# Performance work log

Hardware: AMD Instinct MI355X
Metric: run time of the kernel (lower is better)

The kernel has to match this reference:

```python
import jax, jax.numpy as jnp
import numpy as np

B, L, K, H = 256, 256, 128, 256


def setup_inputs() -> dict:
    key = jax.random.key(0)
    ks = jax.random.split(key, 24)

    def u(k, shape, fan):
        s = 1.0 / np.sqrt(fan)
        return jax.random.uniform(k, shape, minval=-s, maxval=s, dtype=jnp.float32)

    x = jax.random.normal(ks[0], (B, L, K), jnp.float32)
    mask = (jax.random.uniform(ks[1], (B, L, K)) < 0.7).astype(jnp.float32)
    record_num = jax.random.randint(ks[2], (B,), L // 2, L + 1)
    ts = jnp.cumsum(jax.random.uniform(ks[3], (B, L), minval=0.1, maxval=1.0, dtype=jnp.float32), axis=1)
    time_stamp = ts * (jnp.arange(L)[None, :] < record_num[:, None]).astype(jnp.float32)

    return {
        "x": x,
        "mask": mask,
        "time_stamp": time_stamp,
        # TemporalDecay h: W [H,K], stdv = 1/sqrt(out)=1/sqrt(H)
        "W_gh": u(ks[4], (H, K), H), "b_gh": u(ks[5], (H,), H),
        # TemporalDecay x (diag): W [K,K], stdv = 1/sqrt(K)
        "W_gx": u(ks[6], (K, K), K), "b_gx": u(ks[7], (K,), K),
        # hist_reg: Linear(H -> K), stdv = 1/sqrt(H)
        "W_hist": u(ks[8], (K, H), H), "b_hist": u(ks[9], (K,), H),
        "W_feat": u(ks[10], (K, K), K), "b_feat": u(ks[11], (K,), K),
        # weight_combine: Linear(2K -> K), stdv = 1/sqrt(2K)
        "W_comb": u(ks[12], (K, 2 * K), 2 * K), "b_comb": u(ks[13], (K,), 2 * K),
        # GRUCell(2K -> H): uniform 1/sqrt(H)
        "W_ih": u(ks[14], (3 * H, 2 * K), H), "W_hh": u(ks[15], (3 * H, H), H),
        "b_ih": u(ks[16], (3 * H,), H), "b_hh": u(ks[17], (3 * H,), H),
        # out: Linear(H -> 1)
        "W_out": u(ks[18], (1, H), H), "b_out": u(ks[19], (1,), H),
        "record_num": record_num,
        "direct": 0,
    }


def _forward(x, mask, time_stamp, W_gh, b_gh, W_gx, b_gx, W_hist, b_hist,
             W_feat, b_feat, W_comb, b_comb, W_ih, W_hh, b_ih, b_hh,
             W_out, b_out, record_num):
    Bs, Ls, Ks = x.shape
    Hs = W_gh.shape[0]
    eye = jnp.eye(Ks, dtype=x.dtype)
    W_gx_m = W_gx * eye                 # diag temporal decay
    W_feat_m = W_feat * (1.0 - eye)

    # --- deltas (gen_aux_data): d[0]=1; d[t] = |ts[t]-ts[t-1]| + (1-m[t])*d[t-1] ---
    gaps = jnp.abs(jnp.diff(time_stamp, axis=1))          # [B, L-1]
    mask_t = jnp.swapaxes(mask, 0, 1)                     # [L, B, K]

    def dstep(prev, inp):
        gap, m = inp                                      # [B], [B,K]
        d = gap[:, None] + (1.0 - m) * prev
        return d, d

    d0 = jnp.ones((Bs, Ks), x.dtype)
    _, drest = jax.lax.scan(dstep, d0, (gaps.T, mask_t[1:]))
    deltas = jnp.concatenate([d0[None], drest], axis=0)   # [L, B, K]
    valid = (jnp.arange(Ls)[:, None] < record_num[None, :])  # break at record_num
    deltas = jnp.where(valid[:, :, None], deltas, 0.0)

    evals = (time_stamp != 0).astype(x.dtype)             # [B, L]

    x_t = jnp.swapaxes(x, 0, 1)                           # [L, B, K]
    e_t = evals.T                                         # [L, B]

    def step(carry, inp):
        h, xloss = carry
        xt, mt, dt, et = inp                              # [B,K],[B,K],[B,K],[B]
        e_m = et[:, None]
        gamma_h = jnp.exp(-jax.nn.relu(dt @ W_gh.T + b_gh))   # [B,H]
        gamma_x = jnp.exp(-jax.nn.relu(dt @ W_gx_m.T + b_gx)) # [B,K]
        h_prev = h
        h = h * gamma_h
        x_h = h @ W_hist.T + b_hist
        msum = jnp.sum(mt) + 1e-5
        xloss = xloss + jnp.sum(jnp.abs(xt - x_h) * mt) / msum
        x_c = mt * xt + (1.0 - mt) * x_h
        z_h = x_c @ W_feat_m.T + b_feat
        xloss = xloss + jnp.sum(jnp.abs(xt - z_h) * mt * e_m) / msum
        alpha = jnp.concatenate([gamma_x, mt], axis=1) @ W_comb.T + b_comb
        c_h = alpha * z_h + (1.0 - alpha) * x_h
        xloss = xloss + jnp.sum(jnp.abs(xt - c_h) * mt * e_m) / msum
        c_c = mt * xt + (1.0 - mt) * c_h
        inputs = jnp.concatenate([c_c, mt], axis=1)           # [B, 2K]
        gi = inputs @ W_ih.T + b_ih                           # [B, 3H]
        gh = h @ W_hh.T + b_hh
        ir, iz, ig = jnp.split(gi, 3, axis=1)
        hr, hz, hg = jnp.split(gh, 3, axis=1)
        r = jax.nn.sigmoid(ir + hr)
        z = jax.nn.sigmoid(iz + hz)
        n = jnp.tanh(ig + r * hg)
        h_new = (1.0 - z) * n + z * h
        h_new = h_new * e_m + (1.0 - e_m) * h_prev            # freeze h past record
        return (h_new, xloss), c_c * e_m

    h0 = jnp.zeros((Bs, Hs), x.dtype)
    (h_fin, x_loss), imps = jax.lax.scan(step, (h0, jnp.float32(0.0)), (x_t, mask_t, deltas, e_t))
    imputations = jnp.swapaxes(imps, 0, 1)                # [B, L, K]
    predictions = jax.nn.sigmoid(h_fin @ W_out.T + b_out) # [B, 1]
    return imputations, x_loss, predictions


def reference(x, mask, time_stamp, W_gh, b_gh, W_gx, b_gx, W_hist, b_hist,
              W_feat, b_feat, W_comb, b_comb, W_ih, W_hh, b_ih, b_hh,
              W_out, b_out, record_num, direct):
    return _forward(x, mask, time_stamp, W_gh, b_gh, W_gx, b_gx, W_hist, b_hist,
                    W_feat, b_feat, W_comb, b_comb, W_ih, W_hh, b_ih, b_hh,
                    W_out, b_out, record_num)
```

## Files before the change

### kernel.cpp

```cpp
#include <hip/hip_runtime.h>
#include <math.h>

#define BT 256
#define LT 256
#define KT 128
#define HT 256
#define LOSS_IDX ((size_t)BT*LT*KT)
#define PRED_IDX (LOSS_IDX + 1)
#define LDP 1280
#define GH0 0
#define AL0 256
#define GI0 384
#define ZP0 1152

typedef _Float16 h2 __attribute__((ext_vector_type(2)));
typedef _Float16 f16x8 __attribute__((ext_vector_type(8)));
typedef float f32x4 __attribute__((ext_vector_type(4)));

__device__ __forceinline__ float fd2(h2 a, h2 b, float c){
#if __has_builtin(__builtin_amdgcn_fdot2)
  return __builtin_amdgcn_fdot2(a, b, c, false);
#else
  return c + (float)a[0]*(float)b[0] + (float)a[1]*(float)b[1];
#endif
}
__device__ __forceinline__ float dot8(f16x8 w, f16x8 a, float acc){
  acc = fd2(__builtin_shufflevector(w,w,0,1), __builtin_shufflevector(a,a,0,1), acc);
  acc = fd2(__builtin_shufflevector(w,w,2,3), __builtin_shufflevector(a,a,2,3), acc);
  acc = fd2(__builtin_shufflevector(w,w,4,5), __builtin_shufflevector(a,a,4,5), acc);
  acc = fd2(__builtin_shufflevector(w,w,6,7), __builtin_shufflevector(a,a,6,7), acc);
  return acc;
}
__device__ __forceinline__ float sigf(float v){ return 1.0f/(1.0f + __expf(-v)); }
__device__ __forceinline__ float tanh_fast(float v){
  float a = fminf(fabsf(v), 15.0f);
  float e2 = __expf(2.0f*a);
  float r = (e2 - 1.0f)/(e2 + 1.0f);
  return copysignf(r, v);
}
__device__ __forceinline__ float f16bits(unsigned u, int hi){
  union { unsigned short s; _Float16 h; } c;
  c.s = (unsigned short)(hi ? (u >> 16) : (u & 0xffff));
  return (float)c.h;
}

__global__ void pack_cast(const float* __restrict__ src, _Float16* __restrict__ dst,
                          int J, int Kd, int diag, int total){
  int idx = blockIdx.x*256 + threadIdx.x;
  if (idx >= total) return;
  float v = src[idx];
  if (diag && (idx / Kd) == (idx % Kd)) v = 0.0f;
  dst[idx] = (_Float16)v;
}
__global__ void pack_rowchunks(const float* __restrict__ src, _Float16* __restrict__ dst,
                               int J, int K, int total){
  int idx = blockIdx.x*256 + threadIdx.x;
  if (idx >= total) return;
  int j = idx % J, c = idx / J;
  #pragma unroll
  for (int e = 0; e < 8; ++e)
    dst[(size_t)idx*8 + e] = (_Float16)src[(size_t)j*K + c*8 + e];
}
__global__ void pack_col(const float* __restrict__ src, _Float16* __restrict__ dst,
                         int J, int Kc, int ld, int diag, int total){
  int idx = blockIdx.x*256 + threadIdx.x;
  if (idx >= total) return;
  int j = idx % J, k = idx / J;
  float v = src[(size_t)j*ld + k];
  if (diag && j == k) v = 0.0f;
  dst[idx] = (_Float16)v;
}

__global__ __launch_bounds__(128) void scan_kernel(
    const float* __restrict__ x, const float* __restrict__ mask, const float* __restrict__ ts,
    const float* __restrict__ W_gx, const float* __restrict__ b_gx,
    const int* __restrict__ record_num,
    _Float16* __restrict__ deltas, _Float16* __restrict__ Agx, _Float16* __restrict__ U)
{
  int b = blockIdx.x, k = threadIdx.x;
  int rn = record_num[b];
  float gxd = W_gx[(size_t)k*KT + k];
  float bgx = b_gx[k];
  float d = 1.0f, tsp = 0.0f;
  for (int t0 = 0; t0 < LT; t0 += 8){
    float xv[8], mv[8], tsv[8];
    #pragma unroll
    for (int u = 0; u < 8; ++u){
      size_t off = ((size_t)b*LT + t0 + u)*KT + k;
      xv[u] = x[off]; mv[u] = mask[off];
      tsv[u] = ts[(size_t)b*LT + t0 + u];
    }
    #pragma unroll
    for (int u = 0; u < 8; ++u){
      int t = t0 + u;
      if (t > 0){
        float gap = fabsf(tsv[u] - (u ? tsv[u-1] : tsp));
        d = gap + (1.0f - mv[u])*d;
      }
      float e = (t < rn) ? 1.0f : 0.0f;
      float dev = d * e;
      size_t row = (size_t)b*LT + t;
      deltas[row*KT + k] = (_Float16)dev;
      float gx = __expf(-fmaxf(fmaf(dev, gxd, bgx), 0.0f));
      Agx[row*2*KT + k]      = (_Float16)gx;
      Agx[row*2*KT + KT + k] = (_Float16)mv[u];
      U[row*2*KT + k]        = (_Float16)(mv[u]*xv[u]);
      U[row*2*KT + KT + k]   = (_Float16)mv[u];
    }
    tsp = tsv[7];
  }
}

__global__ void msum_kernel(const float* __restrict__ mask, float* __restrict__ msumInv){
  __shared__ float red[256];
  int t = blockIdx.x;
  float acc = 0.0f;
  for (int i = threadIdx.x; i < BT*KT; i += 256){
    int b = i >> 7, k = i & 127;
    acc += mask[((size_t)b*LT + t)*KT + k];
  }
  red[threadIdx.x] = acc; __syncthreads();
  for (int s = 128; s > 0; s >>= 1){
    if (threadIdx.x < s) red[threadIdx.x] += red[threadIdx.x + s];
    __syncthreads();
  }
  if (threadIdx.x == 0) msumInv[t] = 1.0f/(red[0] + 1e-5f);
}

__global__ __launch_bounds__(256) void gemm_f16(
    const _Float16* __restrict__ A, long ldA, int K,
    const _Float16* __restrict__ B, long ldB,
    _Float16* __restrict__ C, long colofs,
    const float* __restrict__ bias, int op)
{
  const int w = threadIdx.x >> 6, lane = threadIdx.x & 63;
  const int ml = lane & 15, quad = lane >> 4;
  const long m0 = (long)blockIdx.x*64 + w*16;
  const long nb0 = (long)blockIdx.y*64;
  f32x4 acc[4] = {{0,0,0,0},{0,0,0,0},{0,0,0,0},{0,0,0,0}};
  for (int kc = 0; kc < K; kc += 32){
    f16x8 a = *(const f16x8*)(A + (m0 + ml)*ldA + kc + quad*8);
    #pragma unroll
    for (int nt = 0; nt < 4; ++nt){
      f16x8 bfr = *(const f16x8*)(B + (nb0 + nt*16 + ml)*ldB + kc + quad*8);
      acc[nt] = __builtin_amdgcn_mfma_f32_16x16x32_f16(a, bfr, acc[nt], 0, 0, 0);
    }
  }
  #pragma unroll
  for (int nt = 0; nt < 4; ++nt){
    long col = nb0 + nt*16 + ml;
    float bv = (op >= 1) ? bias[col] : 0.0f;
    #pragma unroll
    for (int r = 0; r < 4; ++r){
      float v = acc[nt][r];
      if (op >= 1) v += bv;
      if (op == 2) v = __expf(-fmaxf(v, 0.0f));
      long row = m0 + quad*4 + r;
      C[row*LDP + colofs + col] = (_Float16)v;
    }
  }
}

#define NT 768

struct __align__(16) SeqS {
  float h[HT];
  float hs[HT];
  alignas(16) _Float16 hsh[HT];
  float gh[3*HT];
  float gi[3*HT];
  float xh[KT];
  float part[6][KT];
  float v3[KT], v5[KT];
  int lidx[KT];
  int posk[KT];
  int cnt;
  unsigned pb[2][LDP/2];
  float xb[2][KT], mb[2][KT];
  float bhist[KT], bfeat[KT];
  float bhh[3*HT];
  float wout[HT];
  float red[NT/64];
};

__global__ __launch_bounds__(NT, 1) void rits_seq(
    const float* __restrict__ x, const float* __restrict__ mask,
    const int* __restrict__ record_num, const float* __restrict__ msumInv,
    const _Float16* __restrict__ P,
    const f16x8* __restrict__ Whh_p, const f16x8* __restrict__ Whist_p,
    const _Float16* __restrict__ Wfc, const _Float16* __restrict__ Wihc,
    const float* __restrict__ b_hist, const float* __restrict__ b_feat,
    const float* __restrict__ b_hh,
    const float* __restrict__ W_out, const float* __restrict__ b_out,
    float* __restrict__ out)
{
  __shared__ SeqS s;
  const int tid = threadIdx.x;
  const int b = blockIdx.x;
  const int rn = record_num[b];
  const unsigned* __restrict__ Pd = (const unsigned*)P + (size_t)b*LT*(LDP/2);

  if (tid < HT) s.h[tid] = 0.0f;
  if (tid < KT){ s.bhist[tid] = b_hist[tid]; s.bfeat[tid] = b_feat[tid]; }
  if (tid < 3*HT) s.bhh[tid] = b_hh[tid];
  if (tid >= 256 && tid < 512) s.wout[tid - 256] = W_out[tid - 256];
  if (tid < LDP/2) s.pb[0][tid] = Pd[tid];
  else if (tid < LDP/2 + KT){
    int k = tid - LDP/2;
    s.xb[0][k] = x[((size_t)b*LT)*KT + k];
    s.mb[0][k] = mask[((size_t)b*LT)*KT + k];
  }
  __syncthreads();

  float loss = 0.0f;

  for (int t = 0; t < LT; ++t){
    const int cur = t & 1, nxt = cur ^ 1;

    unsigned pr0 = 0; float prx = 0.0f, prm = 0.0f;
    if (t < LT - 1){
      if (tid < LDP/2) pr0 = Pd[(size_t)(t+1)*(LDP/2) + tid];
      else if (tid < LDP/2 + KT){
        int k = tid - LDP/2;
        size_t off = ((size_t)b*LT + t + 1)*KT + k;
        prx = x[off]; prm = mask[off];
      }
    }

    if (tid == 0) s.cnt = 0;
    if (tid < HT){
      float g = f16bits(s.pb[cur][GH0/2 + (tid >> 1)], tid & 1);
      float hsv = s.h[tid] * g;
      s.hs[tid] = hsv;
      s.hsh[tid] = (_Float16)hsv;
    }
    __syncthreads();

    {
      const f16x8* hp = (const f16x8*)s.hsh;
      float acc = 0.0f;
      #pragma unroll 4
      for (int c = 0; c < 32; ++c)
        acc = dot8(Whh_p[c*768 + tid], hp[c], acc);
      s.gh[tid] = acc;
      if (tid < KT){
        float a2 = 0.0f;
        #pragma unroll 4
        for (int c = 0; c < 32; ++c)
          a2 = dot8(Whist_p[c*KT + tid], hp[c], a2);
        float xh = a2 + s.bhist[tid];
        s.xh[tid] = xh;
        float mv = s.mb[cur][tid], xv = s.xb[cur][tid];
        loss += fabsf(xv - xh) * mv * msumInv[t];
        if (mv == 0.0f){
          int pp = atomicAdd(&s.cnt, 1);
          s.lidx[pp] = tid; s.v3[pp] = xh; s.posk[tid] = pp;
        }
      }
    }
    __syncthreads();

    {
      const int st = tid >> 7, j = tid & 127;
      const int c0 = s.cnt;
      float a = 0.0f;
      for (int i = st; i < c0; i += 6)
        a += s.v3[i] * (float)Wfc[s.lidx[i]*KT + j];
      s.part[st][j] = a;
    }
    __syncthreads();
    if (tid < KT){
      const int j = tid;
      float z = f16bits(s.pb[cur][ZP0/2 + (j >> 1)], j & 1) + s.bfeat[j]
              + s.part[0][j] + s.part[1][j] + s.part[2][j]
              + s.part[3][j] + s.part[4][j] + s.part[5][j];
      float al = f16bits(s.pb[cur][AL0/2 + (j >> 1)], j & 1);
      float xh = s.xh[j];
      float mv = s.mb[cur][j], xv = s.xb[cur][j];
      float e = (t < rn) ? 1.0f : 0.0f;
      float inv = msumInv[t];
      float ch = al*z + (1.0f - al)*xh;
      loss += (fabsf(xv - z) + fabsf(xv - ch)) * mv * e * inv;
      float cc = mv*xv + (1.0f - mv)*ch;
      out[((size_t)b*LT + t)*KT + j] = cc * e;
      if (mv == 0.0f) s.v5[s.posk[j]] = ch;
    }
    __syncthreads();

    {
      const int c0 = s.cnt;
      float g = f16bits(s.pb[cur][GI0/2 + (tid >> 1)], tid & 1);
      for (int i = 0; i < c0; ++i)
        g += s.v5[i] * (float)Wihc[s.lidx[i]*768 + tid];
      s.gi[tid] = g;
    }
    __syncthreads();

    if (tid < HT){
      const int j = tid;
      float ir = s.gi[j],        iz = s.gi[HT + j],        ig = s.gi[2*HT + j];
      float hr = s.gh[j] + s.bhh[j];
      float hz = s.gh[HT + j] + s.bhh[HT + j];
      float hg = s.gh[2*HT + j] + s.bhh[2*HT + j];
      float r = sigf(ir + hr);
      float zg = sigf(iz + hz);
      float n = tanh_fast(ig + r*hg);
      float hn = (1.0f - zg)*n + zg*s.hs[j];
      if (t < rn) s.h[j] = hn;
    }
    if (t < LT - 1){
      if (tid < LDP/2) s.pb[nxt][tid] = pr0;
      else if (tid < LDP/2 + KT){
        int k = tid - LDP/2;
        s.xb[nxt][k] = prx; s.mb[nxt][k] = prm;
      }
    }
    __syncthreads();
  }

  #pragma unroll
  for (int off = 32; off; off >>= 1) loss += __shfl_down(loss, off);
  if ((tid & 63) == 0) s.red[tid >> 6] = loss;
  __syncthreads();
  if (tid == 0){
    float tot = 0.0f;
    #pragma unroll
    for (int w = 0; w < NT/64; ++w) tot += s.red[w];
    atomicAdd(&out[LOSS_IDX], tot);
  }

  if (tid < HT) s.part[0][tid & 127] = 0.0f;
  if (tid < HT) s.gh[tid] = s.h[tid] * s.wout[tid];
  __syncthreads();
  for (int st2 = 128; st2 > 0; st2 >>= 1){
    if (tid < st2) s.gh[tid] += s.gh[tid + st2];
    __syncthreads();
  }
  if (tid == 0) out[PRED_IDX + b] = sigf(s.gh[0] + b_out[0]);
}

extern "C" void kernel_launch(void* const* d_in, const int* in_sizes, int n_in,
                              void* d_out, int out_size, void* d_ws, size_t ws_size,
                              hipStream_t stream){
  const float* x      = (const float*)d_in[0];
  const float* mask   = (const float*)d_in[1];
  const float* ts     = (const float*)d_in[2];
  const float* W_gh   = (const float*)d_in[3];
  const float* b_gh   = (const float*)d_in[4];
  const float* W_gx   = (const float*)d_in[5];
  const float* b_gx   = (const float*)d_in[6];
  const float* W_hist = (const float*)d_in[7];
  const float* b_hist = (const float*)d_in[8];
  const float* W_feat = (const float*)d_in[9];
  const float* b_feat = (const float*)d_in[10];
  const float* W_comb = (const float*)d_in[11];
  const float* b_comb = (const float*)d_in[12];
  const float* W_ih   = (const float*)d_in[13];
  const float* W_hh   = (const float*)d_in[14];
  const float* b_ih   = (const float*)d_in[15];
  const float* b_hh   = (const float*)d_in[16];
  const float* W_out  = (const float*)d_in[17];
  const float* b_out  = (const float*)d_in[18];
  const int*   rn     = (const int*)d_in[19];
  float* out = (float*)d_out;
  char* ws = (char*)d_ws;

  size_t off = 0;
  auto alloc = [&](size_t bytes) -> char* {
    char* p = ws + off;
    off += (bytes + 255) & ~(size_t)255;
    return p;
  };
  _Float16* P      = (_Float16*)alloc((size_t)BT*LT*LDP*2);
  _Float16* deltas = (_Float16*)alloc((size_t)BT*LT*KT*2);
  _Float16* Agx    = (_Float16*)alloc((size_t)BT*LT*2*KT*2);
  _Float16* U      = (_Float16*)alloc((size_t)BT*LT*2*KT*2);
  _Float16* WghF   = (_Float16*)alloc(HT*KT*2);
  _Float16* WcombF = (_Float16*)alloc(KT*2*KT*2);
  _Float16* WihF   = (_Float16*)alloc(3*HT*2*KT*2);
  _Float16* WfeatF = (_Float16*)alloc(KT*KT*2);
  _Float16* Whh_p  = (_Float16*)alloc(3*HT*HT*2);
  _Float16* Whist_p= (_Float16*)alloc(KT*HT*2);
  _Float16* Wfc    = (_Float16*)alloc(KT*KT*2);
  _Float16* Wihc   = (_Float16*)alloc(KT*3*HT*2);
  float* msumInv   = (float*)alloc(LT*4);

  auto grid1 = [](int n){ return dim3((n + 255)/256); };
  pack_cast<<<grid1(HT*KT), 256, 0, stream>>>(W_gh, WghF, HT, KT, 0, HT*KT);
  pack_cast<<<grid1(KT*2*KT), 256, 0, stream>>>(W_comb, WcombF, KT, 2*KT, 0, KT*2*KT);
  pack_cast<<<grid1(3*HT*2*KT), 256, 0, stream>>>(W_ih, WihF, 3*HT, 2*KT, 0, 3*HT*2*KT);
  pack_cast<<<grid1(KT*KT), 256, 0, stream>>>(W_feat, WfeatF, KT, KT, 1, KT*KT);
  pack_rowchunks<<<grid1(3*HT*(HT/8)), 256, 0, stream>>>(W_hh, Whh_p, 3*HT, HT, 3*HT*(HT/8));
  pack_rowchunks<<<grid1(KT*(HT/8)), 256, 0, stream>>>(W_hist, Whist_p, KT, HT, KT*(HT/8));
  pack_col<<<grid1(KT*KT), 256, 0, stream>>>(W_feat, Wfc, KT, KT, KT, 1, KT*KT);
  pack_col<<<grid1(768*KT), 256, 0, stream>>>(W_ih, Wihc, 3*HT, KT, 2*KT, 0, 3*HT*KT);

  scan_kernel<<<dim3(BT), dim3(KT), 0, stream>>>(x, mask, ts, W_gx, b_gx, rn, deltas, Agx, U);
  msum_kernel<<<dim3(LT), dim3(256), 0, stream>>>(mask, msumInv);

  const int MR = BT*LT;
  gemm_f16<<<dim3(MR/64, HT/64), 256, 0, stream>>>(deltas, KT, KT, WghF, KT, P, GH0, b_gh, 2);
  gemm_f16<<<dim3(MR/64, KT/64), 256, 0, stream>>>(Agx, 2*KT, 2*KT, WcombF, 2*KT, P, AL0, b_comb, 1);
  gemm_f16<<<dim3(MR/64, 3*HT/64), 256, 0, stream>>>(U, 2*KT, 2*KT, WihF, 2*KT, P, GI0, b_ih, 1);
  gemm_f16<<<dim3(MR/64, KT/64), 256, 0, stream>>>(U, 2*KT, KT, WfeatF, KT, P, ZP0, (const float*)nullptr, 0);

  hipMemsetAsync((void*)(out + LOSS_IDX), 0, sizeof(float), stream);

  rits_seq<<<dim3(BT), dim3(NT), 0, stream>>>(x, mask, rn, msumInv, P,
      (const f16x8*)Whh_p, (const f16x8*)Whist_p, Wfc, Wihc,
      b_hist, b_feat, b_hh, W_out, b_out, out);
}
```

Baseline: 2.581 ms.

## Stage W_hist and W_feat in LDS and prefetch W_ih gather rows early

Copies the packed W_hist (64KB) and the W_feat fp16 matrix (32KB) into shared memory once per block, so the per-timestep hist and feature-regression dot products read LDS instead of global memory. It also caches msumInv in LDS, moves the W_hh matvec after the W_hist work, and prefetches the first 16 masked W_ih rows into registers before a barrier to hide gather latency. The remaining W_ih gather is unrolled by 8 with zero-padded v5 entries. The much larger LDS footprint and extra registers may lower occupancy, though only one block of 768 threads runs per CU anyway.

New measurement: 2.420 ms. 1.07x faster.

```diff
diff --git a/kernel.cpp b/kernel.cpp
--- a/kernel.cpp
+++ b/kernel.cpp
@@ -164,15 +164,17 @@
 #define NT 768
 
 struct __align__(16) SeqS {
+  f16x8 whist_l[32*128];
+  _Float16 wfc_l[128*128];
   float h[HT];
   float hs[HT];
   alignas(16) _Float16 hsh[HT];
   float gh[3*HT];
   float gi[3*HT];
   float xh[KT];
-  float part[6][KT];
+  float part6[6][KT];
   float v3[KT], v5[KT];
-  int lidx[KT];
+  int lidx[136];
   int posk[KT];
   int cnt;
   unsigned pb[2][LDP/2];
@@ -180,6 +182,7 @@
   float bhist[KT], bfeat[KT];
   float bhh[3*HT];
   float wout[HT];
+  float minv[LT];
   float red[NT/64];
 };
 
@@ -200,10 +203,15 @@
   const int rn = record_num[b];
   const unsigned* __restrict__ Pd = (const unsigned*)P + (size_t)b*LT*(LDP/2);
 
+  for (int i = tid; i < 32*128; i += NT) s.whist_l[i] = Whist_p[i];
+  for (int i = tid; i < 128*128/2; i += NT)
+    ((unsigned*)s.wfc_l)[i] = ((const unsigned*)Wfc)[i];
   if (tid < HT) s.h[tid] = 0.0f;
   if (tid < KT){ s.bhist[tid] = b_hist[tid]; s.bfeat[tid] = b_feat[tid]; }
   if (tid < 3*HT) s.bhh[tid] = b_hh[tid];
+  if (tid < 136) s.lidx[tid] = 0;
   if (tid >= 256 && tid < 512) s.wout[tid - 256] = W_out[tid - 256];
+  if (tid >= 512 && tid < 512 + LT) s.minv[tid - 512] = msumInv[tid - 512];
   if (tid < LDP/2) s.pb[0][tid] = Pd[tid];
   else if (tid < LDP/2 + KT){
     int k = tid - LDP/2;
@@ -220,16 +228,15 @@
     unsigned pr0 = 0; float prx = 0.0f, prm = 0.0f;
     if (t < LT - 1){
       if (tid < LDP/2) pr0 = Pd[(size_t)(t+1)*(LDP/2) + tid];
-      else if (tid < LDP/2 + KT){
+      else {
         int k = tid - LDP/2;
-        size_t off = ((size_t)b*LT + t + 1)*KT + k;
-        prx = x[off]; prm = mask[off];
+        size_t offx = ((size_t)b*LT + t + 1)*KT + k;
+        prx = x[offx]; prm = mask[offx];
       }
     }
-
     if (tid == 0) s.cnt = 0;
     if (tid < HT){
-      float g = f16bits(s.pb[cur][GH0/2 + (tid >> 1)], tid & 1);
+      float g = f16bits(s.pb[cur][tid >> 1], tid & 1);
       float hsv = s.h[tid] * g;
       s.hs[tid] = hsv;
       s.hsh[tid] = (_Float16)hsv;
@@ -238,47 +245,54 @@
 
     {
       const f16x8* hp = (const f16x8*)s.hsh;
-      float acc = 0.0f;
-      #pragma unroll 4
-      for (int c = 0; c < 32; ++c)
-        acc = dot8(Whh_p[c*768 + tid], hp[c], acc);
-      s.gh[tid] = acc;
       if (tid < KT){
         float a2 = 0.0f;
-        #pragma unroll 4
+        #pragma unroll 8
         for (int c = 0; c < 32; ++c)
-          a2 = dot8(Whist_p[c*KT + tid], hp[c], a2);
+          a2 = dot8(s.whist_l[c*128 + tid], hp[c], a2);
         float xh = a2 + s.bhist[tid];
         s.xh[tid] = xh;
         float mv = s.mb[cur][tid], xv = s.xb[cur][tid];
-        loss += fabsf(xv - xh) * mv * msumInv[t];
+        loss += fabsf(xv - xh) * mv * s.minv[t];
         if (mv == 0.0f){
           int pp = atomicAdd(&s.cnt, 1);
           s.lidx[pp] = tid; s.v3[pp] = xh; s.posk[tid] = pp;
         }
       }
-    }
-    __syncthreads();
-
+      float acc = 0.0f;
+      #pragma unroll 8
+      for (int c = 0; c < 32; ++c)
+        acc = dot8(Whh_p[c*768 + tid], hp[c], acc);
+      s.gh[tid] = acc;
+    }
+    __syncthreads();
+
+    const int c0 = s.cnt;
+    const int c4 = (c0 + 7) & ~7;
     {
-      const int st = tid >> 7, j = tid & 127;
-      const int c0 = s.cnt;
+      int st = tid >> 7, j = tid & 127;
       float a = 0.0f;
       for (int i = st; i < c0; i += 6)
-        a += s.v3[i] * (float)Wfc[s.lidx[i]*KT + j];
-      s.part[st][j] = a;
-    }
-    __syncthreads();
+        a += s.v3[i] * (float)s.wfc_l[s.lidx[i]*128 + j];
+      s.part6[st][j] = a;
+    }
+    float wpre[16];
+    #pragma unroll
+    for (int u = 0; u < 16; ++u)
+      wpre[u] = (u < c4) ? (float)Wihc[(size_t)s.lidx[u]*768 + tid] : 0.0f;
+    __syncthreads();
+
     if (tid < KT){
       const int j = tid;
+      if (j >= c0 && j < c4) s.v5[j] = 0.0f;
       float z = f16bits(s.pb[cur][ZP0/2 + (j >> 1)], j & 1) + s.bfeat[j]
-              + s.part[0][j] + s.part[1][j] + s.part[2][j]
-              + s.part[3][j] + s.part[4][j] + s.part[5][j];
+              + s.part6[0][j] + s.part6[1][j] + s.part6[2][j]
+              + s.part6[3][j] + s.part6[4][j] + s.part6[5][j];
       float al = f16bits(s.pb[cur][AL0/2 + (j >> 1)], j & 1);
       float xh = s.xh[j];
       float mv = s.mb[cur][j], xv = s.xb[cur][j];
       float e = (t < rn) ? 1.0f : 0.0f;
-      float inv = msumInv[t];
+      float inv = s.minv[t];
       float ch = al*z + (1.0f - al)*xh;
       loss += (fabsf(xv - z) + fabsf(xv - ch)) * mv * e * inv;
       float cc = mv*xv + (1.0f - mv)*ch;
@@ -288,17 +302,22 @@
     __syncthreads();
 
     {
-      const int c0 = s.cnt;
       float g = f16bits(s.pb[cur][GI0/2 + (tid >> 1)], tid & 1);
-      for (int i = 0; i < c0; ++i)
-        g += s.v5[i] * (float)Wihc[s.lidx[i]*768 + tid];
+      #pragma unroll
+      for (int u = 0; u < 16; ++u)
+        if (u < c4) g += s.v5[u] * wpre[u];
+      for (int i = 16; i < c4; i += 8){
+        #pragma unroll
+        for (int u = 0; u < 8; ++u)
+          g += s.v5[i + u] * (float)Wihc[(size_t)s.lidx[i + u]*768 + tid];
+      }
       s.gi[tid] = g;
     }
     __syncthreads();
 
     if (tid < HT){
       const int j = tid;
-      float ir = s.gi[j],        iz = s.gi[HT + j],        ig = s.gi[2*HT + j];
+      float ir = s.gi[j], iz = s.gi[HT + j], ig = s.gi[2*HT + j];
       float hr = s.gh[j] + s.bhh[j];
       float hz = s.gh[HT + j] + s.bhh[HT + j];
       float hg = s.gh[2*HT + j] + s.bhh[2*HT + j];
@@ -310,7 +329,7 @@
     }
     if (t < LT - 1){
       if (tid < LDP/2) s.pb[nxt][tid] = pr0;
-      else if (tid < LDP/2 + KT){
+      else {
         int k = tid - LDP/2;
         s.xb[nxt][k] = prx; s.mb[nxt][k] = prm;
       }
@@ -329,7 +348,6 @@
     atomicAdd(&out[LOSS_IDX], tot);
   }
 
-  if (tid < HT) s.part[0][tid & 127] = 0.0f;
   if (tid < HT) s.gh[tid] = s.h[tid] * s.wout[tid];
   __syncthreads();
   for (int st2 = 128; st2 > 0; st2 >>= 1){
```
